# Performance work log

Hardware: AMD Instinct MI355X
Metric: run time of the kernel (lower is better)

The kernel has to match this reference:

```python
import jax, jax.numpy as jnp
import numpy as np

B, T, D, H = 4, 2048, 1024, 16
Dh = D // H          # 64 head dim
NF = Dh // 2         # 32 rotary frequencies


def setup_inputs() -> dict:
    key = jax.random.key(0)
    k0, k1, k2, k3 = jax.random.split(key, 4)
    x = jax.random.normal(k0, (B, T, D), dtype=jnp.float32)
    # 3D spatial coordinates per token, e.g. voxel positions
    coords = jax.random.uniform(k1, (B, T, 3), dtype=jnp.float32, minval=0.0, maxval=64.0)
    w_scale = 1.0 / np.sqrt(D)
    qkv_w = jax.random.normal(k2, (3 * D, D), dtype=jnp.float32) * w_scale
    qkv_b = jnp.zeros((3 * D,), dtype=jnp.float32)
    proj_w = jax.random.normal(k3, (D, D), dtype=jnp.float32) * w_scale
    proj_b = jnp.zeros((D,), dtype=jnp.float32)
    # mixed-axis rope: frequency f uses coordinate axis (f % 3), geometric period spacing within each axis group
    axes = (jnp.arange(NF) % 3).astype(jnp.int32)
    group = (jnp.arange(NF) // 3).astype(jnp.float32)
    n_per_axis = float(NF) / 3.0
    inv_freq = (10000.0 ** (-group / n_per_axis)).astype(jnp.float32)
    return {"x": x, "coords": coords, "qkv_w": qkv_w, "qkv_b": qkv_b,
            "proj_w": proj_w, "proj_b": proj_b, "inv_freq": inv_freq, "axes": axes}


def _apply_rope(t, sin, cos):
    # t: [B, H, T, Dh]; sin/cos: [B, 1, T, Dh//2]  (rotate-half convention)
    t1, t2 = jnp.split(t, 2, axis=-1)
    return jnp.concatenate([t1 * cos - t2 * sin, t1 * sin + t2 * cos], axis=-1)


def reference(x, coords, qkv_w, qkv_b, proj_w, proj_b, inv_freq, axes):
    b, t, d = x.shape
    # fused QKV projection
    qkv = (x @ qkv_w.T + qkv_b).reshape(b, t, 3, H, Dh)
    qkv = jnp.transpose(qkv, (2, 0, 3, 1, 4))     # [3, B, H, T, Dh]
    q, k, v = qkv[0], qkv[1], qkv[2]
    # vectorized per-sample rope from coords (replaces python loop over batch)
    ang = jnp.take(coords, axes, axis=-1) * inv_freq      # [B, T, NF]
    sin = jnp.sin(ang)[:, None]                            # [B, 1, T, NF]
    cos = jnp.cos(ang)[:, None]
    q = _apply_rope(q, sin, cos)
    k = _apply_rope(k, sin, cos)
    # standard scaling mode: single 1/sqrt(Dh) inside SDPA
    scale = 1.0 / np.sqrt(Dh)
    scores = jnp.einsum('bhqd,bhkd->bhqk', q, k) * scale
    attn = jax.nn.softmax(scores, axis=-1)
    out = jnp.einsum('bhqk,bhkd->bhqd', attn, v)           # [B, H, T, Dh]
    out = jnp.transpose(out, (0, 2, 1, 3)).reshape(b, t, d)
    return out @ proj_w.T + proj_b
```

## Files before the change

### kernel.cpp

```cpp
#include <hip/hip_runtime.h>
#include <hip/hip_bf16.h>

#define B_ 4
#define T_ 2048
#define D_ 1024
#define H_ 16
#define DH 64
#define NF 32
#define BH (B_*H_)
#define M_ROWS (B_*T_)

#define QSCALE 0.125f

using u16 = unsigned short;
using u32 = unsigned int;

typedef __bf16 bf16x8 __attribute__((ext_vector_type(8)));
typedef float  f32x4  __attribute__((ext_vector_type(4)));
typedef float  f32x16 __attribute__((ext_vector_type(16)));

__device__ __forceinline__ u16 f2bf(float f) {
  u32 u = __float_as_uint(f);
  u32 r = u + 0x7fffu + ((u >> 16) & 1u);
  return (u16)(r >> 16);
}
__device__ __forceinline__ u16 f2bf_hw(float f) {
  __bf16 h = (__bf16)f;
  return *(u16*)&h;
}
__device__ __forceinline__ u32 pack2(float lo, float hi) {
  return (u32)f2bf_hw(lo) | ((u32)f2bf_hw(hi) << 16);
}
__device__ __forceinline__ float bf2f(u16 h) {
  return __uint_as_float(((u32)h) << 16);
}

__device__ __forceinline__ void pl32swap(u32 a, u32 b, u32& x, u32& y) {
  x = a; y = b;
  asm("s_nop 1\n\t"
      "v_permlane32_swap_b32 %0, %1"
      : "+v"(x), "+v"(y));
}

__device__ __forceinline__ void gload_lds16(const void* g, void* l) {
  __builtin_amdgcn_global_load_lds((__attribute__((address_space(1))) void*)(g),
                                   (__attribute__((address_space(3))) void*)(l),
                                   16, 0, 0);
}

__global__ __launch_bounds__(256)
void cvt_kernel(const float* __restrict__ in, u16* __restrict__ out, int n8) {
  int idx = blockIdx.x * 256 + threadIdx.x;
  if (idx >= n8) return;
  const float4* p = (const float4*)in + (long)idx * 2;
  float4 a = p[0], b = p[1];
  u32 o0 = (u32)f2bf(a.x) | ((u32)f2bf(a.y) << 16);
  u32 o1 = (u32)f2bf(a.z) | ((u32)f2bf(a.w) << 16);
  u32 o2 = (u32)f2bf(b.x) | ((u32)f2bf(b.y) << 16);
  u32 o3 = (u32)f2bf(b.z) | ((u32)f2bf(b.w) << 16);
  ((uint4*)out)[idx] = make_uint4(o0, o1, o2, o3);
}

__global__ __launch_bounds__(256)
void sincos_kernel(const float* __restrict__ coords, const float* __restrict__ inv_freq,
                   const int* __restrict__ axes, float* __restrict__ sc) {
  int idx = blockIdx.x * 256 + threadIdx.x;
  if (idx >= B_ * T_ * NF) return;
  int f = idx & 31;
  long bt = idx >> 5;
  float c = coords[bt * 3 + axes[f]];
  float ang = c * inv_freq[f];
  sc[bt * 64 + f]      = sinf(ang);
  sc[bt * 64 + 32 + f] = cosf(ang);
}

__global__ __launch_bounds__(256, 2)
void gemm_qkv(const u16* __restrict__ A, const u16* __restrict__ Bt,
              const float* __restrict__ bias, const float* __restrict__ sc,
              u16* __restrict__ qr, u16* __restrict__ kr, u16* __restrict__ vbuf) {
  const int N = 3 * D_, K = D_;
  __shared__ u16 As[128 * 64];
  __shared__ u16 Bs[128 * 64];
  int nb = N >> 7;
  int bid = blockIdx.x;
  int nwg = gridDim.x;
  int cpx = nwg >> 3;
  bid = (bid & 7) * cpx + (bid >> 3);
  int bm = bid / nb, bn = bid % nb;
  long m0 = (long)bm << 7, n0 = (long)bn << 7;
  int tid = threadIdx.x;
  int lane = tid & 63, w = tid >> 6;
  int g = lane >> 4, lr = lane & 15;
  int wm = w >> 1, wn = w & 1;

  f32x4 acc[4][4] = {};

  for (int kt = 0; kt < K; kt += 64) {
    __syncthreads();
    #pragma unroll
    for (int j = 0; j < 4; ++j) {
      int ob = j * 4096 + tid * 16;
      int row = ob >> 7, col = (ob & 127) >> 1;
      u16* ldsA = As + j * 2048 + w * 512;
      u16* ldsB = Bs + j * 2048 + w * 512;
      gload_lds16(A + (m0 + row) * K + kt + col, ldsA);
      gload_lds16(Bt + (n0 + row) * K + kt + col, ldsB);
    }
    __syncthreads();
    #pragma unroll
    for (int kk = 0; kk < 2; ++kk) {
      bf16x8 af[4], bfr[4];
      #pragma unroll
      for (int i = 0; i < 4; ++i)
        af[i] = *(const bf16x8*)(As + (wm * 64 + i * 16 + lr) * 64 + kk * 32 + g * 8);
      #pragma unroll
      for (int i = 0; i < 4; ++i)
        bfr[i] = *(const bf16x8*)(Bs + (wn * 64 + i * 16 + lr) * 64 + kk * 32 + g * 8);
      #pragma unroll
      for (int mi = 0; mi < 4; ++mi)
        #pragma unroll
        for (int nj = 0; nj < 4; ++nj)
          acc[mi][nj] = __builtin_amdgcn_mfma_f32_16x16x32_bf16(af[mi], bfr[nj], acc[mi][nj], 0, 0, 0);
    }
  }

  int part = (int)(n0 >> 10);
  int h = ((int)(n0 & 1023) >> 6) + wn;
  float bv[4];
  #pragma unroll
  for (int nj = 0; nj < 4; ++nj)
    bv[nj] = bias[n0 + wn * 64 + nj * 16 + lr];

  #pragma unroll
  for (int mi = 0; mi < 4; ++mi) {
    #pragma unroll
    for (int i = 0; i < 4; ++i) {
      long row = m0 + wm * 64 + mi * 16 + g * 4 + i;
      int b = (int)(row >> 11), t = (int)(row & 2047);
      long obase = ((long)(b * 16 + h) * T_ + t) * 64;
      if (part == 2) {
        #pragma unroll
        for (int nj = 0; nj < 4; ++nj)
          vbuf[obase + nj * 16 + lr] = f2bf(acc[mi][nj][i] + bv[nj]);
      } else {
        u16* outp = part ? kr : qr;
        float fac = part ? 1.0f : QSCALE;
        const float* scp = sc + row * 64;
        #pragma unroll
        for (int nj = 0; nj < 2; ++nj) {
          int d = nj * 16 + lr;
          float sn = scp[d], cs = scp[32 + d];
          float t1 = acc[mi][nj][i]     + bv[nj];
          float t2 = acc[mi][nj + 2][i] + bv[nj + 2];
          outp[obase + d]      = f2bf((t1 * cs - t2 * sn) * fac);
          outp[obase + 32 + d] = f2bf((t1 * sn + t2 * cs) * fac);
        }
      }
    }
  }
}

__global__ __launch_bounds__(256, 2)
void gemm_bt(const u16* __restrict__ A, const u16* __restrict__ Bt,
             const float* __restrict__ bias, float* __restrict__ Cout,
             int M, int N, int K) {
  __shared__ u16 As[128 * 64];
  __shared__ u16 Bs[128 * 64];
  int nb = N >> 7;
  int bid = blockIdx.x;
  int nwg = gridDim.x;
  if ((nwg & 7) == 0) {
    int c = nwg >> 3;
    bid = (bid & 7) * c + (bid >> 3);
  }
  int bm = bid / nb, bn = bid % nb;
  long m0 = (long)bm << 7, n0 = (long)bn << 7;
  int tid = threadIdx.x;
  int lane = tid & 63, w = tid >> 6;
  int g = lane >> 4, lr = lane & 15;
  int wm = w >> 1, wn = w & 1;

  f32x4 acc[4][4] = {};

  for (int kt = 0; kt < K; kt += 64) {
    __syncthreads();
    #pragma unroll
    for (int j = 0; j < 4; ++j) {
      int ob = j * 4096 + tid * 16;
      int row = ob >> 7, col = (ob & 127) >> 1;
      u16* ldsA = As + j * 2048 + w * 512;
      u16* ldsB = Bs + j * 2048 + w * 512;
      gload_lds16(A + (m0 + row) * K + kt + col, ldsA);
      gload_lds16(Bt + (n0 + row) * K + kt + col, ldsB);
    }
    __syncthreads();
    #pragma unroll
    for (int kk = 0; kk < 2; ++kk) {
      bf16x8 af[4], bfr[4];
      #pragma unroll
      for (int i = 0; i < 4; ++i)
        af[i] = *(const bf16x8*)(As + (wm * 64 + i * 16 + lr) * 64 + kk * 32 + g * 8);
      #pragma unroll
      for (int i = 0; i < 4; ++i)
        bfr[i] = *(const bf16x8*)(Bs + (wn * 64 + i * 16 + lr) * 64 + kk * 32 + g * 8);
      #pragma unroll
      for (int mi = 0; mi < 4; ++mi)
        #pragma unroll
        for (int nj = 0; nj < 4; ++nj)
          acc[mi][nj] = __builtin_amdgcn_mfma_f32_16x16x32_bf16(af[mi], bfr[nj], acc[mi][nj], 0, 0, 0);
    }
  }
  #pragma unroll
  for (int mi = 0; mi < 4; ++mi) {
    #pragma unroll
    for (int nj = 0; nj < 4; ++nj) {
      long col = n0 + wn * 64 + nj * 16 + lr;
      float bvv = bias[col];
      #pragma unroll
      for (int i = 0; i < 4; ++i) {
        long row = m0 + wm * 64 + mi * 16 + g * 4 + i;
        Cout[row * (long)N + col] = acc[mi][nj][i] + bvv;
      }
    }
  }
}

__global__ __launch_bounds__(256)
void vtrans_kernel(const u16* __restrict__ vbuf, u16* __restrict__ vt) {
  __shared__ u16 Vsm[128 * 72];
  int bh = blockIdx.y;
  int t0 = blockIdx.x << 7;
  int tid = threadIdx.x;
  #pragma unroll
  for (int it = 0; it < 4; ++it) {
    int item = it * 256 + tid;
    int tl = item >> 3, dg = item & 7;
    uint4 u = *(const uint4*)(vbuf + ((long)bh * T_ + t0 + tl) * 64 + dg * 8);
    *(uint4*)(Vsm + tl * 72 + dg * 8) = u;
  }
  __syncthreads();
  int d = tid >> 2, tc = tid & 3;
  long obase = ((long)bh * DH + d) * T_ + t0 + tc * 32;
  #pragma unroll
  for (int c = 0; c < 4; ++c) {
    u32 o[4];
    #pragma unroll
    for (int j = 0; j < 4; ++j) {
      u16 lo = Vsm[(tc * 32 + c * 8 + 2 * j)     * 72 + d];
      u16 hi = Vsm[(tc * 32 + c * 8 + 2 * j + 1) * 72 + d];
      o[j] = (u32)lo | ((u32)hi << 16);
    }
    *(uint4*)(vt + obase + c * 8) = make_uint4(o[0], o[1], o[2], o[3]);
  }
}

__global__ __launch_bounds__(256, 4)
void attn_kernel(const u16* __restrict__ Qr, const u16* __restrict__ Kr,
                 const u16* __restrict__ Vt, u16* __restrict__ Aout) {
  __shared__ u16 Ks[2][64 * 64];
  __shared__ u16 Vs[2][64 * 64];
  int wg = (blockIdx.x & 7) * 128 + (blockIdx.x >> 3);
  int bh = wg >> 4;
  int b = bh >> 4, h = bh & 15;
  int q0 = (wg & 15) << 7;
  int tid = threadIdx.x;
  int lane = tid & 63, w = tid >> 6;
  int l5 = lane & 31, hb = lane >> 5;

  const long tbase = (long)bh * T_;
  const long vbase = (long)bh * DH;

  bf16x8 bq[4];
  #pragma unroll
  for (int s = 0; s < 4; ++s)
    bq[s] = *(const bf16x8*)(Qr + (tbase + q0 + w * 32 + l5) * DH + s * 16 + hb * 8);

  f32x16 oacc0 = {}, oacc1 = {};
  float lsum = 0.f;

  const int sl = l5 & 7;

  auto STAGE = [&](int buf, int kb) {
    #pragma unroll
    for (int j = 0; j < 2; ++j) {
      int ob = j * 4096 + tid * 16;
      int row = ob >> 7;
      int c = ((ob >> 4) & 7) ^ (row & 7);
      u16* ldsK = Ks[buf] + j * 2048 + w * 512;
      u16* ldsV = Vs[buf] + j * 2048 + w * 512;
      gload_lds16(Kr + (tbase + kb + row) * DH + c * 8, ldsK);
      gload_lds16(Vt + (vbase + row) * T_ + kb + c * 8, ldsV);
    }
  };

  STAGE(0, 0);
  asm volatile("s_waitcnt vmcnt(0)" ::: "memory");
  __builtin_amdgcn_s_barrier();
  __builtin_amdgcn_sched_barrier(0);

  int cur = 0;
  for (int kt = 0; kt < T_ / 64; ++kt) {
    if (kt + 1 < T_ / 64) STAGE(cur ^ 1, (kt + 1) * 64);

    const u16* kbuf = Ks[cur];
    const u16* vbuf = Vs[cur];

    f32x16 p0 = {}, p1 = {};
    #pragma unroll
    for (int s = 0; s < 4; ++s) {
      int c = ((2 * s + hb) ^ sl) * 8;
      bf16x8 ak0 = *(const bf16x8*)(kbuf + l5 * 64 + c);
      bf16x8 ak1 = *(const bf16x8*)(kbuf + (32 + l5) * 64 + c);
      p0 = __builtin_amdgcn_mfma_f32_32x32x16_bf16(ak0, bq[s], p0, 0, 0, 0);
      p1 = __builtin_amdgcn_mfma_f32_32x32x16_bf16(ak1, bq[s], p1, 0, 0, 0);
    }

    u32 pA[8], pB[8];
    #pragma unroll
    for (int r4 = 0; r4 < 4; ++r4) {
      float a0 = __expf(p0[4 * r4 + 0]);
      float a1 = __expf(p0[4 * r4 + 1]);
      float a2 = __expf(p0[4 * r4 + 2]);
      float a3 = __expf(p0[4 * r4 + 3]);
      lsum += (a0 + a1) + (a2 + a3);
      pA[r4] = pack2(a0, a1);
      pB[r4] = pack2(a2, a3);
      float b0 = __expf(p1[4 * r4 + 0]);
      float b1 = __expf(p1[4 * r4 + 1]);
      float b2 = __expf(p1[4 * r4 + 2]);
      float b3 = __expf(p1[4 * r4 + 3]);
      lsum += (b0 + b1) + (b2 + b3);
      pA[4 + r4] = pack2(b0, b1);
      pB[4 + r4] = pack2(b2, b3);
    }

    #pragma unroll
    for (int s2 = 0; s2 < 4; ++s2) {
      u32 w0, w2, w1, w3;
      pl32swap(pA[2 * s2], pA[2 * s2 + 1], w0, w2);
      pl32swap(pB[2 * s2], pB[2 * s2 + 1], w1, w3);
      union { u32 u[4]; bf16x8 v; } bw;
      bw.u[0] = w0; bw.u[1] = w1; bw.u[2] = w2; bw.u[3] = w3;
      int c = ((2 * s2 + hb) ^ sl) * 8;
      bf16x8 av0 = *(const bf16x8*)(vbuf + l5 * 64 + c);
      bf16x8 av1 = *(const bf16x8*)(vbuf + (32 + l5) * 64 + c);
      oacc0 = __builtin_amdgcn_mfma_f32_32x32x16_bf16(av0, bw.v, oacc0, 0, 0, 0);
      oacc1 = __builtin_amdgcn_mfma_f32_32x32x16_bf16(av1, bw.v, oacc1, 0, 0, 0);
    }

    __builtin_amdgcn_sched_barrier(0);
    asm volatile("s_waitcnt vmcnt(0)" ::: "memory");
    __builtin_amdgcn_s_barrier();
    __builtin_amdgcn_sched_barrier(0);
    cur ^= 1;
  }

  lsum += __shfl_xor(lsum, 32);
  float inv = 1.0f / lsum;
  long row = (long)b * T_ + q0 + w * 32 + l5;
  u16* ob = Aout + row * D_ + h * DH;
  #pragma unroll
  for (int r4 = 0; r4 < 4; ++r4) {
    u32 w0 = pack2(oacc0[4 * r4 + 0] * inv, oacc0[4 * r4 + 1] * inv);
    u32 w1 = pack2(oacc0[4 * r4 + 2] * inv, oacc0[4 * r4 + 3] * inv);
    *(uint2*)(ob + r4 * 8 + hb * 4) = make_uint2(w0, w1);
    u32 w2 = pack2(oacc1[4 * r4 + 0] * inv, oacc1[4 * r4 + 1] * inv);
    u32 w3 = pack2(oacc1[4 * r4 + 2] * inv, oacc1[4 * r4 + 3] * inv);
    *(uint2*)(ob + 32 + r4 * 8 + hb * 4) = make_uint2(w2, w3);
  }
}

extern "C" void kernel_launch(void* const* d_in, const int* in_sizes, int n_in,
                              void* d_out, int out_size, void* d_ws, size_t ws_size,
                              hipStream_t stream) {
  const float* x        = (const float*)d_in[0];
  const float* coords   = (const float*)d_in[1];
  const float* qkv_w    = (const float*)d_in[2];
  const float* qkv_b    = (const float*)d_in[3];
  const float* proj_w   = (const float*)d_in[4];
  const float* proj_b   = (const float*)d_in[5];
  const float* inv_freq = (const float*)d_in[6];
  const int*   axes     = (const int*)d_in[7];
  float* out = (float*)d_out;

  char* ws = (char*)d_ws;
  size_t off = 0;
  auto alloc = [&](size_t bytes) -> char* {
    char* p = ws + off;
    off += (bytes + 255) & ~(size_t)255;
    return p;
  };
  u16*   xb     = (u16*)  alloc((size_t)M_ROWS * D_ * 2);
  u16*   wqkv   = (u16*)  alloc((size_t)3 * D_ * D_ * 2);
  u16*   wproj  = (u16*)  alloc((size_t)D_ * D_ * 2);
  float* sc     = (float*)alloc((size_t)M_ROWS * 64 * 4);
  u16*   qr     = (u16*)  alloc((size_t)BH * T_ * DH * 2);
  u16*   kr     = (u16*)  alloc((size_t)BH * T_ * DH * 2);
  u16*   vbuf   = (u16*)  alloc((size_t)BH * T_ * DH * 2);
  u16*   vt     = (u16*)  alloc((size_t)BH * T_ * DH * 2);
  u16*   aout   = vbuf;

  cvt_kernel<<<(M_ROWS * D_ / 8 + 255) / 256, 256, 0, stream>>>(x, xb, M_ROWS * D_ / 8);
  cvt_kernel<<<(3 * D_ * D_ / 8 + 255) / 256, 256, 0, stream>>>(qkv_w, wqkv, 3 * D_ * D_ / 8);
  cvt_kernel<<<(D_ * D_ / 8 + 255) / 256, 256, 0, stream>>>(proj_w, wproj, D_ * D_ / 8);
  sincos_kernel<<<(B_ * T_ * NF + 255) / 256, 256, 0, stream>>>(coords, inv_freq, axes, sc);

  gemm_qkv<<<(M_ROWS / 128) * (3 * D_ / 128), 256, 0, stream>>>(xb, wqkv, qkv_b, sc,
                                                                qr, kr, vbuf);
  vtrans_kernel<<<dim3(T_ / 128, BH), 256, 0, stream>>>(vbuf, vt);
  attn_kernel<<<1024, 256, 0, stream>>>(qr, kr, vt, aout);
  gemm_bt<<<(M_ROWS / 128) * (D_ / 128), 256, 0, stream>>>(aout, wproj, proj_b, out,
                                                           M_ROWS, D_, D_);
}
```

Baseline: 223.8 us.

## Process 64 query rows per wave in attention to reuse K/V fragments

Each wave in the attention kernel now handles two 32-row query subtiles (256 queries per workgroup) instead of one. Every K and V fragment read from LDS feeds twice as many MFMAs, and each K/V tile staged from global memory serves twice as many queries. The grid halves to 512 workgroups and launch bounds drop to 2 blocks per SM, trading occupancy and register pressure for less LDS and global traffic per unit of compute.

```diff
diff --git a/kernel.cpp b/kernel.cpp
--- a/kernel.cpp
+++ b/kernel.cpp
@@ -254,29 +254,33 @@
   }
 }
 
-__global__ __launch_bounds__(256, 4)
+__global__ __launch_bounds__(256, 2)
 void attn_kernel(const u16* __restrict__ Qr, const u16* __restrict__ Kr,
                  const u16* __restrict__ Vt, u16* __restrict__ Aout) {
   __shared__ u16 Ks[2][64 * 64];
   __shared__ u16 Vs[2][64 * 64];
-  int wg = (blockIdx.x & 7) * 128 + (blockIdx.x >> 3);
-  int bh = wg >> 4;
+  int wg = (blockIdx.x & 7) * 64 + (blockIdx.x >> 3);
+  int bh = wg >> 3;
   int b = bh >> 4, h = bh & 15;
-  int q0 = (wg & 15) << 7;
+  int q0 = (wg & 7) << 8;
   int tid = threadIdx.x;
   int lane = tid & 63, w = tid >> 6;
   int l5 = lane & 31, hb = lane >> 5;
 
   const long tbase = (long)bh * T_;
   const long vbase = (long)bh * DH;
-
-  bf16x8 bq[4];
-  #pragma unroll
-  for (int s = 0; s < 4; ++s)
-    bq[s] = *(const bf16x8*)(Qr + (tbase + q0 + w * 32 + l5) * DH + s * 16 + hb * 8);
-
-  f32x16 oacc0 = {}, oacc1 = {};
-  float lsum = 0.f;
+  const int qs = q0 + w * 64;
+
+  bf16x8 bq0[4], bq1[4];
+  #pragma unroll
+  for (int s = 0; s < 4; ++s) {
+    bq0[s] = *(const bf16x8*)(Qr + (tbase + qs + l5)      * DH + s * 16 + hb * 8);
+    bq1[s] = *(const bf16x8*)(Qr + (tbase + qs + 32 + l5) * DH + s * 16 + hb * 8);
+  }
+
+  f32x16 oa00 = {}, oa01 = {};
+  f32x16 oa10 = {}, oa11 = {};
+  float ls0 = 0.f, ls1 = 0.f;
 
   const int sl = l5 & 7;
 
@@ -305,47 +309,57 @@
     const u16* kbuf = Ks[cur];
     const u16* vbuf = Vs[cur];
 
-    f32x16 p0 = {}, p1 = {};
+    f32x16 p00 = {}, p01 = {}, p10 = {}, p11 = {};
     #pragma unroll
     for (int s = 0; s < 4; ++s) {
       int c = ((2 * s + hb) ^ sl) * 8;
       bf16x8 ak0 = *(const bf16x8*)(kbuf + l5 * 64 + c);
       bf16x8 ak1 = *(const bf16x8*)(kbuf + (32 + l5) * 64 + c);
-      p0 = __builtin_amdgcn_mfma_f32_32x32x16_bf16(ak0, bq[s], p0, 0, 0, 0);
-      p1 = __builtin_amdgcn_mfma_f32_32x32x16_bf16(ak1, bq[s], p1, 0, 0, 0);
-    }
-
-    u32 pA[8], pB[8];
+      p00 = __builtin_amdgcn_mfma_f32_32x32x16_bf16(ak0, bq0[s], p00, 0, 0, 0);
+      p01 = __builtin_amdgcn_mfma_f32_32x32x16_bf16(ak1, bq0[s], p01, 0, 0, 0);
+      p10 = __builtin_amdgcn_mfma_f32_32x32x16_bf16(ak0, bq1[s], p10, 0, 0, 0);
+      p11 = __builtin_amdgcn_mfma_f32_32x32x16_bf16(ak1, bq1[s], p11, 0, 0, 0);
+    }
+
+    u32 pA0[8], pB0[8], pA1[8], pB1[8];
     #pragma unroll
     for (int r4 = 0; r4 < 4; ++r4) {
-      float a0 = __expf(p0[4 * r4 + 0]);
-      float a1 = __expf(p0[4 * r4 + 1]);
-      float a2 = __expf(p0[4 * r4 + 2]);
-      float a3 = __expf(p0[4 * r4 + 3]);
-      lsum += (a0 + a1) + (a2 + a3);
-      pA[r4] = pack2(a0, a1);
-      pB[r4] = pack2(a2, a3);
-      float b0 = __expf(p1[4 * r4 + 0]);
-      float b1 = __expf(p1[4 * r4 + 1]);
-      float b2 = __expf(p1[4 * r4 + 2]);
-      float b3 = __expf(p1[4 * r4 + 3]);
-      lsum += (b0 + b1) + (b2 + b3);
-      pA[4 + r4] = pack2(b0, b1);
-      pB[4 + r4] = pack2(b2, b3);
+      float a0 = __expf(p00[4 * r4 + 0]), a1 = __expf(p00[4 * r4 + 1]);
+      float a2 = __expf(p00[4 * r4 + 2]), a3 = __expf(p00[4 * r4 + 3]);
+      ls0 += (a0 + a1) + (a2 + a3);
+      pA0[r4] = pack2(a0, a1); pB0[r4] = pack2(a2, a3);
+      float b0 = __expf(p01[4 * r4 + 0]), b1 = __expf(p01[4 * r4 + 1]);
+      float b2 = __expf(p01[4 * r4 + 2]), b3 = __expf(p01[4 * r4 + 3]);
+      ls0 += (b0 + b1) + (b2 + b3);
+      pA0[4 + r4] = pack2(b0, b1); pB0[4 + r4] = pack2(b2, b3);
+      float c0 = __expf(p10[4 * r4 + 0]), c1 = __expf(p10[4 * r4 + 1]);
+      float c2 = __expf(p10[4 * r4 + 2]), c3 = __expf(p10[4 * r4 + 3]);
+      ls1 += (c0 + c1) + (c2 + c3);
+      pA1[r4] = pack2(c0, c1); pB1[r4] = pack2(c2, c3);
+      float d0 = __expf(p11[4 * r4 + 0]), d1 = __expf(p11[4 * r4 + 1]);
+      float d2 = __expf(p11[4 * r4 + 2]), d3 = __expf(p11[4 * r4 + 3]);
+      ls1 += (d0 + d1) + (d2 + d3);
+      pA1[4 + r4] = pack2(d0, d1); pB1[4 + r4] = pack2(d2, d3);
     }
 
     #pragma unroll
     for (int s2 = 0; s2 < 4; ++s2) {
-      u32 w0, w2, w1, w3;
-      pl32swap(pA[2 * s2], pA[2 * s2 + 1], w0, w2);
-      pl32swap(pB[2 * s2], pB[2 * s2 + 1], w1, w3);
-      union { u32 u[4]; bf16x8 v; } bw;
-      bw.u[0] = w0; bw.u[1] = w1; bw.u[2] = w2; bw.u[3] = w3;
       int c = ((2 * s2 + hb) ^ sl) * 8;
       bf16x8 av0 = *(const bf16x8*)(vbuf + l5 * 64 + c);
       bf16x8 av1 = *(const bf16x8*)(vbuf + (32 + l5) * 64 + c);
-      oacc0 = __builtin_amdgcn_mfma_f32_32x32x16_bf16(av0, bw.v, oacc0, 0, 0, 0);
-      oacc1 = __builtin_amdgcn_mfma_f32_32x32x16_bf16(av1, bw.v, oacc1, 0, 0, 0);
+      u32 w0, w1, w2, w3;
+      pl32swap(pA0[2 * s2], pA0[2 * s2 + 1], w0, w2);
+      pl32swap(pB0[2 * s2], pB0[2 * s2 + 1], w1, w3);
+      union { u32 u[4]; bf16x8 v; } bw0;
+      bw0.u[0] = w0; bw0.u[1] = w1; bw0.u[2] = w2; bw0.u[3] = w3;
+      oa00 = __builtin_amdgcn_mfma_f32_32x32x16_bf16(av0, bw0.v, oa00, 0, 0, 0);
+      oa01 = __builtin_amdgcn_mfma_f32_32x32x16_bf16(av1, bw0.v, oa01, 0, 0, 0);
+      pl32swap(pA1[2 * s2], pA1[2 * s2 + 1], w0, w2);
+      pl32swap(pB1[2 * s2], pB1[2 * s2 + 1], w1, w3);
+      union { u32 u[4]; bf16x8 v; } bw1;
+      bw1.u[0] = w0; bw1.u[1] = w1; bw1.u[2] = w2; bw1.u[3] = w3;
+      oa10 = __builtin_amdgcn_mfma_f32_32x32x16_bf16(av0, bw1.v, oa10, 0, 0, 0);
+      oa11 = __builtin_amdgcn_mfma_f32_32x32x16_bf16(av1, bw1.v, oa11, 0, 0, 0);
     }
 
     __builtin_amdgcn_sched_barrier(0);
@@ -355,18 +369,27 @@
     cur ^= 1;
   }
 
-  lsum += __shfl_xor(lsum, 32);
-  float inv = 1.0f / lsum;
-  long row = (long)b * T_ + q0 + w * 32 + l5;
-  u16* ob = Aout + row * D_ + h * DH;
+  ls0 += __shfl_xor(ls0, 32);
+  ls1 += __shfl_xor(ls1, 32);
+  float inv0 = 1.0f / ls0;
+  float inv1 = 1.0f / ls1;
+  long row0 = (long)b * T_ + qs + l5;
+  u16* ob0 = Aout + row0 * D_ + h * DH;
+  u16* ob1 = ob0 + 32 * D_;
   #pragma unroll
   for (int r4 = 0; r4 < 4; ++r4) {
-    u32 w0 = pack2(oacc0[4 * r4 + 0] * inv, oacc0[4 * r4 + 1] * inv);
-    u32 w1 = pack2(oacc0[4 * r4 + 2] * inv, oacc0[4 * r4 + 3] * inv);
-    *(uint2*)(ob + r4 * 8 + hb * 4) = make_uint2(w0, w1);
-    u32 w2 = pack2(oacc1[4 * r4 + 0] * inv, oacc1[4 * r4 + 1] * inv);
-    u32 w3 = pack2(oacc1[4 * r4 + 2] * inv, oacc1[4 * r4 + 3] * inv);
-    *(uint2*)(ob + 32 + r4 * 8 + hb * 4) = make_uint2(w2, w3);
+    u32 w0 = pack2(oa00[4 * r4 + 0] * inv0, oa00[4 * r4 + 1] * inv0);
+    u32 w1 = pack2(oa00[4 * r4 + 2] * inv0, oa00[4 * r4 + 3] * inv0);
+    *(uint2*)(ob0 + r4 * 8 + hb * 4) = make_uint2(w0, w1);
+    u32 w2 = pack2(oa01[4 * r4 + 0] * inv0, oa01[4 * r4 + 1] * inv0);
+    u32 w3 = pack2(oa01[4 * r4 + 2] * inv0, oa01[4 * r4 + 3] * inv0);
+    *(uint2*)(ob0 + 32 + r4 * 8 + hb * 4) = make_uint2(w2, w3);
+    u32 w4 = pack2(oa10[4 * r4 + 0] * inv1, oa10[4 * r4 + 1] * inv1);
+    u32 w5 = pack2(oa10[4 * r4 + 2] * inv1, oa10[4 * r4 + 3] * inv1);
+    *(uint2*)(ob1 + r4 * 8 + hb * 4) = make_uint2(w4, w5);
+    u32 w6 = pack2(oa11[4 * r4 + 0] * inv1, oa11[4 * r4 + 1] * inv1);
+    u32 w7 = pack2(oa11[4 * r4 + 2] * inv1, oa11[4 * r4 + 3] * inv1);
+    *(uint2*)(ob1 + 32 + r4 * 8 + hb * 4) = make_uint2(w6, w7);
   }
 }
 
@@ -408,7 +431,7 @@
   gemm_qkv<<<(M_ROWS / 128) * (3 * D_ / 128), 256, 0, stream>>>(xb, wqkv, qkv_b, sc,
                                                                 qr, kr, vbuf);
   vtrans_kernel<<<dim3(T_ / 128, BH), 256, 0, stream>>>(vbuf, vt);
-  attn_kernel<<<1024, 256, 0, stream>>>(qr, kr, vt, aout);
+  attn_kernel<<<512, 256, 0, stream>>>(qr, kr, vt, aout);
   gemm_bt<<<(M_ROWS / 128) * (D_ / 128), 256, 0, stream>>>(aout, wproj, proj_b, out,
                                                            M_ROWS, D_, D_);
 }
```

Measured after the change: 214.4 us. 1.04x faster.
